# Optimization experiments

Measured on AMD Instinct MI355X. Metric: run time of the kernel, lower is better.

## Reference

```python
import jax, jax.numpy as jnp
import numpy as np

B, H, S, D = 2, 16, 2048, 64

def setup_inputs() -> dict:
    key = jax.random.key(0)
    kq, kk, kv = jax.random.split(key, 3)
    q = jax.random.normal(kq, (B, H, S, D), dtype=jnp.float32)
    k = jax.random.normal(kk, (B, H, S, D), dtype=jnp.float32)
    v = jax.random.normal(kv, (B, H, S, D), dtype=jnp.float32)
    # additive causal mask: 0 on/below diagonal, -1e9 above
    causal = jnp.tril(jnp.ones((S, S), dtype=bool))
    mask = jnp.where(causal, 0.0, -1e9).astype(jnp.float32)[None, None]
    return {"q": q, "k": k, "v": v, "mask": mask}

def reference(q, k, v, mask):
    # scores: [B,H,Sq,Sk]
    scale = 1.0 / jnp.sqrt(jnp.asarray(k.shape[-1], dtype=q.dtype))
    scores = jnp.einsum("bhqd,bhkd->bhqk", q, k) * scale
    scores = scores + mask
    attn = jax.nn.softmax(scores, axis=-1)
    return jnp.einsum("bhqk,bhkd->bhqd", attn, v)
```

## Files before the change

### kernel.cpp

```cpp
#include <hip/hip_runtime.h>
#include <hip/hip_bf16.h>


#define S_LEN 2048
#define D_DIM 64
#define BKV 64
#define NBH 32
#define NT128 16

typedef __bf16 bf16x8 __attribute__((ext_vector_type(8)));
typedef __bf16 bf16x4 __attribute__((ext_vector_type(4)));
typedef float f32x4 __attribute__((ext_vector_type(4)));

#define QSCALE 0.1803368801111243f
#define NEG_MASK (-1e30f)
#define M_INIT  (-1e29f)
#define THRLOG2 11.5f

__device__ inline void glds16(const void* g, void* l) {
    __builtin_amdgcn_global_load_lds(
        (const __attribute__((address_space(1))) unsigned int*)g,
        (__attribute__((address_space(3))) unsigned int*)l, 16, 0, 0);
}

__device__ inline float m3(float a, float b, float c) {
    return fmaxf(fmaxf(a, b), c);
}

__global__ __launch_bounds__(256)
void conv_fused_kernel(const float* __restrict__ k, const float* __restrict__ v,
                       __bf16* __restrict__ kb, __bf16* __restrict__ vt)
{
    __shared__ __bf16 T[64][72];
    const int bh = blockIdx.y, st = blockIdx.x;
    const int tid = threadIdx.x;
    const size_t base = (size_t)bh * S_LEN * D_DIM + (size_t)st * 64 * D_DIM;
    const float* kh = k + base;
    const float* vh = v + base;
    __bf16* kbh = kb + base;

#pragma unroll
    for (int it = 0; it < 2; ++it) {
        size_t i = ((size_t)tid + it * 256) * 8;
        float4 a = *(const float4*)(kh + i);
        float4 b = *(const float4*)(kh + i + 4);
        bf16x8 o;
        o[0] = (__bf16)a.x; o[1] = (__bf16)a.y; o[2] = (__bf16)a.z; o[3] = (__bf16)a.w;
        o[4] = (__bf16)b.x; o[5] = (__bf16)b.y; o[6] = (__bf16)b.z; o[7] = (__bf16)b.w;
        *(bf16x8*)(kbh + i) = o;
    }

#pragma unroll
    for (int it = 0; it < 4; ++it) {
        int idx = tid + it * 256;
        int s = idx >> 4, c4 = idx & 15;
        float4 f = *(const float4*)(vh + s * D_DIM + c4 * 4);
        T[c4 * 4 + 0][s] = (__bf16)f.x;
        T[c4 * 4 + 1][s] = (__bf16)f.y;
        T[c4 * 4 + 2][s] = (__bf16)f.z;
        T[c4 * 4 + 3][s] = (__bf16)f.w;
    }
    __syncthreads();
    __bf16* vth = vt + (size_t)bh * D_DIM * S_LEN + st * 64;
#pragma unroll
    for (int it = 0; it < 2; ++it) {
        int idx = tid + it * 256;
        int d = idx >> 3, c8 = idx & 7;
        int kk = c8 >> 2, g = c8 & 3;
        bf16x4 v0 = *(const bf16x4*)&T[d][kk * 32 + 4 * g];
        bf16x4 v1 = *(const bf16x4*)&T[d][kk * 32 + 16 + 4 * g];
        bf16x8 o;
        o[0] = v0[0]; o[1] = v0[1]; o[2] = v0[2]; o[3] = v0[3];
        o[4] = v1[0]; o[5] = v1[1]; o[6] = v1[2]; o[7] = v1[3];
        *(bf16x8*)(vth + (size_t)d * S_LEN + c8 * 8) = o;
    }
}


#define STAGE(kt, buf)                                                          \
    {                                                                           \
        _Pragma("unroll")                                                       \
        for (int u = 0; u < 2; ++u) {                                           \
            glds16(kh + (size_t)((kt) * BKV + row_u[u]) * D_DIM + scol_u[u],    \
                   (__bf16*)&KL[buf][0][0] + (u * 4 + w) * 512);                \
            glds16(vh + (size_t)row_u[u] * S_LEN + (kt) * BKV + scol_u[u],      \
                   (__bf16*)&VL[buf][0][0] + (u * 4 + w) * 512);                \
        }                                                                       \
    }


__global__ __launch_bounds__(256, 4)
void attn_fwd_split(const float* __restrict__ q, const __bf16* __restrict__ kb,
                    const __bf16* __restrict__ vt, __bf16* __restrict__ opart,
                    float* __restrict__ ml)
{
    __shared__ __bf16 KL[2][64][64];
    __shared__ __bf16 VL[2][64][64];

    const int tid  = threadIdx.x;
    const int w    = tid >> 6;
    const int lane = tid & 63;
    const int l15  = lane & 15;
    const int lg   = lane >> 4;

    const int u0 = blockIdx.x;
    const int T  = NT128 - 1 - (u0 >> 1);
    const int h  = u0 & 1;
    const int bh = blockIdx.y;
    const int qbase = T * 128;
    const int cnt   = T + 1;

    const float*  qh = q  + (size_t)bh * S_LEN * D_DIM;
    const __bf16* kh = kb + (size_t)bh * S_LEN * D_DIM;
    const __bf16* vh = vt + (size_t)bh * D_DIM * S_LEN;

    int row_u[2], scol_u[2];
#pragma unroll
    for (int u = 0; u < 2; ++u) {
        int e = (u * 4 + w) * 512 + lane * 8;
        int r = e >> 6, c0 = e & 63;
        row_u[u]  = r;
        scol_u[u] = c0 ^ ((r & 7) << 3);
    }

    bf16x8 qf[2][2];
#pragma unroll
    for (int qc = 0; qc < 2; ++qc) {
        const int qrow = qbase + w * 32 + qc * 16 + l15;
        const float* qp = qh + (size_t)qrow * D_DIM + 8 * lg;
#pragma unroll
        for (int kk = 0; kk < 2; ++kk) {
            float4 a = *(const float4*)(qp + kk * 32);
            float4 b = *(const float4*)(qp + kk * 32 + 4);
            bf16x8 f;
            f[0] = (__bf16)(a.x * QSCALE); f[1] = (__bf16)(a.y * QSCALE);
            f[2] = (__bf16)(a.z * QSCALE); f[3] = (__bf16)(a.w * QSCALE);
            f[4] = (__bf16)(b.x * QSCALE); f[5] = (__bf16)(b.y * QSCALE);
            f[6] = (__bf16)(b.z * QSCALE); f[7] = (__bf16)(b.w * QSCALE);
            qf[qc][kk] = f;
        }
    }

    f32x4 acc[4][2] = {};
    float m_run[2]  = {M_INIT, M_INIT};
    float l_part[2] = {0.0f, 0.0f};

    STAGE(h, 0);

    for (int i = 0; i < cnt; ++i) {
        const int kt  = h + 2 * i;
        const int cur = i & 1;
        asm volatile("s_waitcnt vmcnt(0)" ::: "memory");
        __builtin_amdgcn_s_barrier();
        if (i + 1 < cnt) STAGE(kt + 2, cur ^ 1);

        bf16x8 kf[4][2];
#pragma unroll
        for (int jt = 0; jt < 4; ++jt) {
            const int j  = jt * 16 + l15;
            const int sw = (j & 7) << 3;
            kf[jt][0] = *(const bf16x8*)&KL[cur][j][(8 * lg) ^ sw];
            kf[jt][1] = *(const bf16x8*)&KL[cur][j][(32 + 8 * lg) ^ sw];
        }

        f32x4 s0[4], s1[4];
        __builtin_amdgcn_s_setprio(1);
#pragma unroll
        for (int jt = 0; jt < 4; ++jt) {
            f32x4 c = {};
            c = __builtin_amdgcn_mfma_f32_16x16x32_bf16(kf[jt][0], qf[0][0], c, 0, 0, 0);
            c = __builtin_amdgcn_mfma_f32_16x16x32_bf16(kf[jt][1], qf[0][1], c, 0, 0, 0);
            s0[jt] = c;
            f32x4 d = {};
            d = __builtin_amdgcn_mfma_f32_16x16x32_bf16(kf[jt][0], qf[1][0], d, 0, 0, 0);
            d = __builtin_amdgcn_mfma_f32_16x16x32_bf16(kf[jt][1], qf[1][1], d, 0, 0, 0);
            s1[jt] = d;
        }
        __builtin_amdgcn_s_setprio(0);

        if (i == cnt - 1) {
            const int q0 = w * 32 + l15;
#pragma unroll
            for (int jt = 0; jt < 4; ++jt)
#pragma unroll
                for (int r = 0; r < 4; ++r) {
                    const int jl = h * 64 + jt * 16 + 4 * lg + r;
                    if (jl > q0)      s0[jt][r] = NEG_MASK;
                    if (jl > q0 + 16) s1[jt][r] = NEG_MASK;
                }
        }

        float mxl0, mxl1;
        {
            float t0 = m3(s0[0][0], s0[0][1], s0[0][2]);
            float t1 = m3(s0[0][3], s0[1][0], s0[1][1]);
            float t2 = m3(s0[1][2], s0[1][3], s0[2][0]);
            float t3 = m3(s0[2][1], s0[2][2], s0[2][3]);
            float t4 = m3(s0[3][0], s0[3][1], s0[3][2]);
            mxl0 = m3(m3(t0, t1, t2), m3(t3, t4, s0[3][3]), NEG_MASK);
            float u1 = m3(s1[0][0], s1[0][1], s1[0][2]);
            float u2 = m3(s1[0][3], s1[1][0], s1[1][1]);
            float u3 = m3(s1[1][2], s1[1][3], s1[2][0]);
            float u4 = m3(s1[2][1], s1[2][2], s1[2][3]);
            float u5 = m3(s1[3][0], s1[3][1], s1[3][2]);
            mxl1 = m3(m3(u1, u2, u3), m3(u4, u5, s1[3][3]), NEG_MASK);
        }

        if (__any((mxl0 > m_run[0] + THRLOG2) || (mxl1 > m_run[1] + THRLOG2))) {
            float mx0 = fmaxf(mxl0, __shfl_xor(mxl0, 16));
            mx0 = fmaxf(mx0, __shfl_xor(mx0, 32));
            float mx1 = fmaxf(mxl1, __shfl_xor(mxl1, 16));
            mx1 = fmaxf(mx1, __shfl_xor(mx1, 32));
            const float mt0 = fmaxf(m_run[0], mx0);
            const float mt1 = fmaxf(m_run[1], mx1);
            const float c0 = __builtin_amdgcn_exp2f(m_run[0] - mt0);
            const float c1 = __builtin_amdgcn_exp2f(m_run[1] - mt1);
            l_part[0] *= c0; m_run[0] = mt0;
            l_part[1] *= c1; m_run[1] = mt1;
            float ca0[4], ca1[4];
#pragma unroll
            for (int r = 0; r < 4; ++r) {
                ca0[r] = __shfl(c0, 4 * lg + r);
                ca1[r] = __shfl(c1, 4 * lg + r);
            }
#pragma unroll
            for (int dt = 0; dt < 4; ++dt)
#pragma unroll
                for (int r = 0; r < 4; ++r) {
                    acc[dt][0][r] *= ca0[r];
                    acc[dt][1][r] *= ca1[r];
                }
        }

        float ps0 = 0.0f, ps1 = 0.0f;
        bf16x8 pa0[2], pa1[2];
#pragma unroll
        for (int kk = 0; kk < 2; ++kk)
#pragma unroll
            for (int i2 = 0; i2 < 4; ++i2) {
                float ea = __builtin_amdgcn_exp2f(s0[2 * kk][i2] - m_run[0]);
                float eb = __builtin_amdgcn_exp2f(s0[2 * kk + 1][i2] - m_run[0]);
                ps0 += ea + eb;
                pa0[kk][i2]     = (__bf16)ea;
                pa0[kk][4 + i2] = (__bf16)eb;
                float fa = __builtin_amdgcn_exp2f(s1[2 * kk][i2] - m_run[1]);
                float fb = __builtin_amdgcn_exp2f(s1[2 * kk + 1][i2] - m_run[1]);
                ps1 += fa + fb;
                pa1[kk][i2]     = (__bf16)fa;
                pa1[kk][4 + i2] = (__bf16)fb;
            }
        l_part[0] += ps0;
        l_part[1] += ps1;

        __builtin_amdgcn_s_setprio(1);
#pragma unroll
        for (int dt = 0; dt < 4; ++dt) {
            const int d  = dt * 16 + l15;
            const int sw = (d & 7) << 3;
#pragma unroll
            for (int kk = 0; kk < 2; ++kk) {
                bf16x8 vb = *(const bf16x8*)&VL[cur][d][(kk * 32 + 8 * lg) ^ sw];
                acc[dt][0] = __builtin_amdgcn_mfma_f32_16x16x32_bf16(pa0[kk], vb, acc[dt][0], 0, 0, 0);
                acc[dt][1] = __builtin_amdgcn_mfma_f32_16x16x32_bf16(pa1[kk], vb, acc[dt][1], 0, 0, 0);
            }
        }
        __builtin_amdgcn_s_setprio(0);
    }

    __bf16* op  = opart + ((((size_t)bh * NT128 + T) * 2 + h) << 13);
    float*  mlp = ml    + ((((size_t)bh * NT128 + T) * 2 + h) << 8);
#pragma unroll
    for (int qc = 0; qc < 2; ++qc) {
        float lt = l_part[qc] + __shfl_xor(l_part[qc], 16);
        lt += __shfl_xor(lt, 32);
#pragma unroll
        for (int dt = 0; dt < 4; ++dt)
#pragma unroll
            for (int r = 0; r < 4; ++r)
                op[(w * 32 + qc * 16 + 4 * lg + r) * 64 + dt * 16 + l15] =
                    (__bf16)acc[dt][qc][r];
        if (lg == 0) {
            mlp[w * 32 + qc * 16 + l15]       = m_run[qc];
            mlp[128 + w * 32 + qc * 16 + l15] = lt;
        }
    }
}


__global__ __launch_bounds__(256)
void combine_kernel(const __bf16* __restrict__ opart, const float* __restrict__ ml,
                    float* __restrict__ out)
{
    const int T   = blockIdx.x;
    const int bh  = blockIdx.y;
    const int tid = threadIdx.x;
    const int row = tid >> 1;
    const int c0  = (tid & 1) * 32;

    const float* mlp = ml + (((size_t)bh * NT128 + T) * 2 << 8);
    const float m0 = mlp[row],       l0 = mlp[128 + row];
    const float m1 = mlp[256 + row], l1 = mlp[384 + row];
    const float M  = fmaxf(m0, m1);
    const float w0 = __builtin_amdgcn_exp2f(m0 - M);
    const float w1 = __builtin_amdgcn_exp2f(m1 - M);
    const float li = __builtin_amdgcn_rcpf(w0 * l0 + w1 * l1);

    const __bf16* o0 = opart + (((size_t)bh * NT128 + T) * 2 << 13) + row * 64 + c0;
    const __bf16* o1 = o0 + 8192;
    float* oh = out + ((size_t)bh * S_LEN + T * 128 + row) * D_DIM + c0;
#pragma unroll
    for (int cc = 0; cc < 4; ++cc) {
        bf16x8 a = *(const bf16x8*)(o0 + cc * 8);
        bf16x8 b = *(const bf16x8*)(o1 + cc * 8);
        float4 r0, r1;
        r0.x = ((float)a[0] * w0 + (float)b[0] * w1) * li;
        r0.y = ((float)a[1] * w0 + (float)b[1] * w1) * li;
        r0.z = ((float)a[2] * w0 + (float)b[2] * w1) * li;
        r0.w = ((float)a[3] * w0 + (float)b[3] * w1) * li;
        r1.x = ((float)a[4] * w0 + (float)b[4] * w1) * li;
        r1.y = ((float)a[5] * w0 + (float)b[5] * w1) * li;
        r1.z = ((float)a[6] * w0 + (float)b[6] * w1) * li;
        r1.w = ((float)a[7] * w0 + (float)b[7] * w1) * li;
        ((float4*)(oh + cc * 8))[0] = r0;
        ((float4*)(oh + cc * 8))[1] = r1;
    }
}


__global__ __launch_bounds__(256)
void attn_fwd_glds(const float* __restrict__ q, const __bf16* __restrict__ kb,
                   const __bf16* __restrict__ vt, float* __restrict__ out)
{
    __shared__ __bf16 KL[3][64][64];
    __shared__ __bf16 VL[3][64][64];

    const int tid  = threadIdx.x;
    const int w    = tid >> 6;
    const int lane = tid & 63;
    const int l15  = lane & 15;
    const int lg   = lane >> 4;

    const int p  = blockIdx.x;
    const int bh = blockIdx.y;

    const float*  qh = q  + (size_t)bh * S_LEN * D_DIM;
    const __bf16* kh = kb + (size_t)bh * S_LEN * D_DIM;
    const __bf16* vh = vt + (size_t)bh * D_DIM * S_LEN;
    float*        oh = out + (size_t)bh * S_LEN * D_DIM;

    int row_u[2], scol_u[2];
#pragma unroll
    for (int u = 0; u < 2; ++u) {
        int e = (u * 4 + w) * 512 + lane * 8;
        int r = e >> 6, c0 = e & 63;
        row_u[u]  = r;
        scol_u[u] = c0 ^ ((r & 7) << 3);
    }

    for (int half = 0; half < 2; ++half) {
        const int qtile = (half == 0) ? (31 - p) : p;
        const int qbase = qtile * 64;
        const int nt    = qtile + 1;

        bf16x8 qf[2];
        {
            const int qrow = qbase + w * 16 + l15;
            const float* qp = qh + (size_t)qrow * D_DIM + 8 * lg;
#pragma unroll
            for (int kk = 0; kk < 2; ++kk) {
                float4 a = *(const float4*)(qp + kk * 32);
                float4 b = *(const float4*)(qp + kk * 32 + 4);
                bf16x8 f;
                f[0] = (__bf16)(a.x * QSCALE); f[1] = (__bf16)(a.y * QSCALE);
                f[2] = (__bf16)(a.z * QSCALE); f[3] = (__bf16)(a.w * QSCALE);
                f[4] = (__bf16)(b.x * QSCALE); f[5] = (__bf16)(b.y * QSCALE);
                f[6] = (__bf16)(b.z * QSCALE); f[7] = (__bf16)(b.w * QSCALE);
                qf[kk] = f;
            }
        }

        f32x4 acc[4] = {};
        float m_run = M_INIT;
        float l_part = 0.0f;

        if (half == 1) __syncthreads();
        STAGE(0, 0);
        if (nt > 1) STAGE(1, 1);

        for (int kt = 0; kt < nt; ++kt) {
            const int cur = kt % 3;
            if (kt + 1 < nt) { asm volatile("s_waitcnt vmcnt(4)" ::: "memory"); }
            else             { asm volatile("s_waitcnt vmcnt(0)" ::: "memory"); }
            __builtin_amdgcn_s_barrier();
            if (kt + 2 < nt) STAGE(kt + 2, (kt + 2) % 3);

            f32x4 s[4];
            __builtin_amdgcn_s_setprio(1);
#pragma unroll
            for (int jt = 0; jt < 4; ++jt) {
                const int j  = jt * 16 + l15;
                const int sw = (j & 7) << 3;
                f32x4 c = {};
#pragma unroll
                for (int kk = 0; kk < 2; ++kk) {
                    bf16x8 kf = *(const bf16x8*)&KL[cur][j][(kk * 32 + 8 * lg) ^ sw];
                    c = __builtin_amdgcn_mfma_f32_16x16x32_bf16(kf, qf[kk], c, 0, 0, 0);
                }
                s[jt] = c;
// ... 163 lines not shown
            sfrag[kc] = c;
        }

        if (kt == qtile) {
#pragma unroll
            for (int kc = 0; kc < 4; ++kc) {
                const int j = kv0 + kc * 16 + l15;
#pragma unroll
                for (int r = 0; r < 4; ++r) {
                    const int qrow = qbase + w * 16 + lg * 4 + r;
                    if (j > qrow) sfrag[kc][r] = -1e30f;
                }
            }
        }

        float mt[4], corr[4], ps[4];
#pragma unroll
        for (int r = 0; r < 4; ++r) {
            float mx = fmaxf(fmaxf(sfrag[0][r], sfrag[1][r]),
                             fmaxf(sfrag[2][r], sfrag[3][r]));
            mx = fmaxf(mx, __shfl_xor(mx, 1));
            mx = fmaxf(mx, __shfl_xor(mx, 2));
            mx = fmaxf(mx, __shfl_xor(mx, 4));
            mx = fmaxf(mx, __shfl_xor(mx, 8));
            mt[r]   = fmaxf(m_run[r], mx);
            corr[r] = __expf(m_run[r] - mt[r]);
            ps[r]   = 0.0f;
        }
#pragma unroll
        for (int kc = 0; kc < 4; ++kc) {
#pragma unroll
            for (int r = 0; r < 4; ++r) {
                float pp = __expf(sfrag[kc][r] - mt[r]);
                ps[r] += pp;
                Plds[w][lg * 4 + r][kc * 16 + l15] = (__bf16)pp;
            }
        }
#pragma unroll
        for (int r = 0; r < 4; ++r) {
            ps[r] += __shfl_xor(ps[r], 1);
            ps[r] += __shfl_xor(ps[r], 2);
            ps[r] += __shfl_xor(ps[r], 4);
            ps[r] += __shfl_xor(ps[r], 8);
            l_run[r] = l_run[r] * corr[r] + ps[r];
            m_run[r] = mt[r];
        }
#pragma unroll
        for (int dt = 0; dt < 4; ++dt)
#pragma unroll
            for (int r = 0; r < 4; ++r)
                acc[dt][r] *= corr[r];

#pragma unroll
        for (int kk = 0; kk < 2; ++kk) {
            bf16x8 pf = *(const bf16x8*)&Plds[w][l15][kk * 32 + 8 * lg];
#pragma unroll
            for (int dt = 0; dt < 4; ++dt) {
                bf16x8 vf = *(const bf16x8*)&Vt[dt * 16 + l15][kk * 32 + 8 * lg];
                acc[dt] = __builtin_amdgcn_mfma_f32_16x16x32_bf16(pf, vf, acc[dt], 0, 0, 0);
            }
        }
    }

#pragma unroll
    for (int dt = 0; dt < 4; ++dt) {
#pragma unroll
        for (int r = 0; r < 4; ++r) {
            const int qrow = qbase + w * 16 + lg * 4 + r;
            oh[(size_t)qrow * D_DIM + dt * 16 + l15] = acc[dt][r] / l_run[r];
        }
    }
}

extern "C" void kernel_launch(void* const* d_in, const int* in_sizes, int n_in,
                              void* d_out, int out_size, void* d_ws, size_t ws_size,
                              hipStream_t stream) {
    const float* q = (const float*)d_in[0];
    const float* k = (const float*)d_in[1];
    const float* v = (const float*)d_in[2];
    float* out = (float*)d_out;

    const size_t kv_elems   = (size_t)NBH * S_LEN * D_DIM;
    const size_t conv_bytes = kv_elems * 2 * sizeof(__bf16);
    const size_t op_bytes   = (size_t)NBH * NT128 * 2 * 8192 * 2;
    const size_t ml_bytes   = (size_t)NBH * NT128 * 2 * 256 * 4;

    if (ws_size >= conv_bytes + op_bytes + ml_bytes) {
        __bf16* kb = (__bf16*)d_ws;
        __bf16* vt = kb + kv_elems;
        __bf16* opart = (__bf16*)((char*)d_ws + conv_bytes);
        float*  ml    = (float*)((char*)d_ws + conv_bytes + op_bytes);
        conv_fused_kernel<<<dim3(S_LEN / 64, NBH), dim3(256), 0, stream>>>(k, v, kb, vt);
        attn_fwd_split<<<dim3(32, NBH), dim3(256), 0, stream>>>(q, kb, vt, opart, ml);
        combine_kernel<<<dim3(NT128, NBH), dim3(256), 0, stream>>>(opart, ml, out);
    } else if (ws_size >= conv_bytes) {
        __bf16* kb = (__bf16*)d_ws;
        __bf16* vt = kb + kv_elems;
        conv_fused_kernel<<<dim3(S_LEN / 64, NBH), dim3(256), 0, stream>>>(k, v, kb, vt);
        attn_fwd_glds<<<dim3(16, NBH), dim3(256), 0, stream>>>(q, kb, vt, out);
    } else {
        attn_fwd_fallback<<<dim3(S_LEN / 64, NBH), dim3(256), 0, stream>>>(q, k, v, out);
    }
}
```

Measured before the change: 65.00 us.

## Split KV four ways and pair mirrored query tiles per block for balance

The split-KV attention kernel now divides each query tile's causal key range into four interleaved chunks instead of two. Each block walks two query tiles in turn, a long one (15-p) and a short one (p), so causal work is spread evenly across blocks and the longest block finishes sooner. The causal mask now applies to any diagonal key tile rather than only the last iteration, and the combine kernel merges four partial results per row. In exchange, the bf16 partial-output and max/sum workspace doubles, which adds global memory traffic and needs a larger workspace. If the workspace is too small, the code drops to the slower fallback path.

After: 88.69 us. +36.5%, slower.

```diff
diff --git a/kernel.cpp b/kernel.cpp
--- a/kernel.cpp
+++ b/kernel.cpp
@@ -104,11 +104,9 @@
     const int lg   = lane >> 4;
 
     const int u0 = blockIdx.x;
-    const int T  = NT128 - 1 - (u0 >> 1);
-    const int h  = u0 & 1;
+    const int p  = u0 >> 2;
+    const int h  = u0 & 3;
     const int bh = blockIdx.y;
-    const int qbase = T * 128;
-    const int cnt   = T + 1;
 
     const float*  qh = q  + (size_t)bh * S_LEN * D_DIM;
     const __bf16* kh = kb + (size_t)bh * S_LEN * D_DIM;
@@ -123,165 +121,173 @@
         scol_u[u] = c0 ^ ((r & 7) << 3);
     }
 
-    bf16x8 qf[2][2];
-#pragma unroll
-    for (int qc = 0; qc < 2; ++qc) {
-        const int qrow = qbase + w * 32 + qc * 16 + l15;
-        const float* qp = qh + (size_t)qrow * D_DIM + 8 * lg;
-#pragma unroll
-        for (int kk = 0; kk < 2; ++kk) {
-            float4 a = *(const float4*)(qp + kk * 32);
-            float4 b = *(const float4*)(qp + kk * 32 + 4);
-            bf16x8 f;
-            f[0] = (__bf16)(a.x * QSCALE); f[1] = (__bf16)(a.y * QSCALE);
-            f[2] = (__bf16)(a.z * QSCALE); f[3] = (__bf16)(a.w * QSCALE);
-            f[4] = (__bf16)(b.x * QSCALE); f[5] = (__bf16)(b.y * QSCALE);
-            f[6] = (__bf16)(b.z * QSCALE); f[7] = (__bf16)(b.w * QSCALE);
-            qf[qc][kk] = f;
-        }
-    }
-
-    f32x4 acc[4][2] = {};
-    float m_run[2]  = {M_INIT, M_INIT};
-    float l_part[2] = {0.0f, 0.0f};
-
-    STAGE(h, 0);
-
-    for (int i = 0; i < cnt; ++i) {
-        const int kt  = h + 2 * i;
-        const int cur = i & 1;
-        asm volatile("s_waitcnt vmcnt(0)" ::: "memory");
-        __builtin_amdgcn_s_barrier();
-        if (i + 1 < cnt) STAGE(kt + 2, cur ^ 1);
-
-        bf16x8 kf[4][2];
-#pragma unroll
-        for (int jt = 0; jt < 4; ++jt) {
-            const int j  = jt * 16 + l15;
-            const int sw = (j & 7) << 3;
-            kf[jt][0] = *(const bf16x8*)&KL[cur][j][(8 * lg) ^ sw];
-            kf[jt][1] = *(const bf16x8*)&KL[cur][j][(32 + 8 * lg) ^ sw];
-        }
-
-        f32x4 s0[4], s1[4];
-        __builtin_amdgcn_s_setprio(1);
-#pragma unroll
-        for (int jt = 0; jt < 4; ++jt) {
-            f32x4 c = {};
-            c = __builtin_amdgcn_mfma_f32_16x16x32_bf16(kf[jt][0], qf[0][0], c, 0, 0, 0);
-            c = __builtin_amdgcn_mfma_f32_16x16x32_bf16(kf[jt][1], qf[0][1], c, 0, 0, 0);
-            s0[jt] = c;
-            f32x4 d = {};
-            d = __builtin_amdgcn_mfma_f32_16x16x32_bf16(kf[jt][0], qf[1][0], d, 0, 0, 0);
-            d = __builtin_amdgcn_mfma_f32_16x16x32_bf16(kf[jt][1], qf[1][1], d, 0, 0, 0);
-            s1[jt] = d;
-        }
-        __builtin_amdgcn_s_setprio(0);
-
-        if (i == cnt - 1) {
-            const int q0 = w * 32 + l15;
-#pragma unroll
-            for (int jt = 0; jt < 4; ++jt)
+    for (int chain = 0; chain < 2; ++chain) {
+        const int T     = (chain == 0) ? (NT128 - 1 - p) : p;
+        const int qbase = T * 128;
+        const int cnt   = (2 * T + 1 >= h) ? ((2 * T + 1 - h) >> 2) + 1 : 0;
+
+        bf16x8 qf[2][2];
+#pragma unroll
+        for (int qc = 0; qc < 2; ++qc) {
+            const int qrow = qbase + w * 32 + qc * 16 + l15;
+            const float* qp = qh + (size_t)qrow * D_DIM + 8 * lg;
+#pragma unroll
+            for (int kk = 0; kk < 2; ++kk) {
+                float4 a = *(const float4*)(qp + kk * 32);
+                float4 b = *(const float4*)(qp + kk * 32 + 4);
+                bf16x8 f;
+                f[0] = (__bf16)(a.x * QSCALE); f[1] = (__bf16)(a.y * QSCALE);
+                f[2] = (__bf16)(a.z * QSCALE); f[3] = (__bf16)(a.w * QSCALE);
+                f[4] = (__bf16)(b.x * QSCALE); f[5] = (__bf16)(b.y * QSCALE);
+                f[6] = (__bf16)(b.z * QSCALE); f[7] = (__bf16)(b.w * QSCALE);
+                qf[qc][kk] = f;
+            }
+        }
+
+        f32x4 acc[4][2] = {};
+        float m_run[2]  = {M_INIT, M_INIT};
+        float l_part[2] = {0.0f, 0.0f};
+
+        if (chain == 1) __syncthreads();
+        if (cnt > 0) STAGE(h, 0);
+
+        for (int i = 0; i < cnt; ++i) {
+            const int kt  = h + 4 * i;
+            const int cur = i & 1;
+            asm volatile("s_waitcnt vmcnt(0)" ::: "memory");
+            __builtin_amdgcn_s_barrier();
+            if (i + 1 < cnt) STAGE(kt + 4, cur ^ 1);
+
+            bf16x8 kf[4][2];
+#pragma unroll
+            for (int jt = 0; jt < 4; ++jt) {
+                const int j  = jt * 16 + l15;
+                const int sw = (j & 7) << 3;
+                kf[jt][0] = *(const bf16x8*)&KL[cur][j][(8 * lg) ^ sw];
+                kf[jt][1] = *(const bf16x8*)&KL[cur][j][(32 + 8 * lg) ^ sw];
+            }
+
+            f32x4 s0[4], s1[4];
+            __builtin_amdgcn_s_setprio(1);
+#pragma unroll
+            for (int jt = 0; jt < 4; ++jt) {
+                f32x4 c = {};
+                c = __builtin_amdgcn_mfma_f32_16x16x32_bf16(kf[jt][0], qf[0][0], c, 0, 0, 0);
+                c = __builtin_amdgcn_mfma_f32_16x16x32_bf16(kf[jt][1], qf[0][1], c, 0, 0, 0);
+                s0[jt] = c;
+                f32x4 d = {};
+                d = __builtin_amdgcn_mfma_f32_16x16x32_bf16(kf[jt][0], qf[1][0], d, 0, 0, 0);
+                d = __builtin_amdgcn_mfma_f32_16x16x32_bf16(kf[jt][1], qf[1][1], d, 0, 0, 0);
+                s1[jt] = d;
+            }
+            __builtin_amdgcn_s_setprio(0);
+
+            if (kt >= 2 * T) {
+                const int dj = (kt - 2 * T) * 64;
+                const int q0 = w * 32 + l15;
+#pragma unroll
+                for (int jt = 0; jt < 4; ++jt)
+#pragma unroll
+                    for (int r = 0; r < 4; ++r) {
+                        const int jl = dj + jt * 16 + 4 * lg + r;
+                        if (jl > q0)      s0[jt][r] = NEG_MASK;
+                        if (jl > q0 + 16) s1[jt][r] = NEG_MASK;
+                    }
+            }
+
+            float mxl0, mxl1;
+            {
+                float t0 = m3(s0[0][0], s0[0][1], s0[0][2]);
+                float t1 = m3(s0[0][3], s0[1][0], s0[1][1]);
+                float t2 = m3(s0[1][2], s0[1][3], s0[2][0]);
+                float t3 = m3(s0[2][1], s0[2][2], s0[2][3]);
+                float t4 = m3(s0[3][0], s0[3][1], s0[3][2]);
+                mxl0 = m3(m3(t0, t1, t2), m3(t3, t4, s0[3][3]), NEG_MASK);
+                float u1 = m3(s1[0][0], s1[0][1], s1[0][2]);
+                float u2 = m3(s1[0][3], s1[1][0], s1[1][1]);
+                float u3 = m3(s1[1][2], s1[1][3], s1[2][0]);
+                float u4 = m3(s1[2][1], s1[2][2], s1[2][3]);
+                float u5 = m3(s1[3][0], s1[3][1], s1[3][2]);
+                mxl1 = m3(m3(u1, u2, u3), m3(u4, u5, s1[3][3]), NEG_MASK);
+            }
+
+            if (__any((mxl0 > m_run[0] + THRLOG2) || (mxl1 > m_run[1] + THRLOG2))) {
+                float mx0 = fmaxf(mxl0, __shfl_xor(mxl0, 16));
+                mx0 = fmaxf(mx0, __shfl_xor(mx0, 32));
+                float mx1 = fmaxf(mxl1, __shfl_xor(mxl1, 16));
+                mx1 = fmaxf(mx1, __shfl_xor(mx1, 32));
+                const float mt0 = fmaxf(m_run[0], mx0);
+                const float mt1 = fmaxf(m_run[1], mx1);
+                const float c0 = __builtin_amdgcn_exp2f(m_run[0] - mt0);
+                const float c1 = __builtin_amdgcn_exp2f(m_run[1] - mt1);
+                l_part[0] *= c0; m_run[0] = mt0;
+                l_part[1] *= c1; m_run[1] = mt1;
+                float ca0[4], ca1[4];
 #pragma unroll
                 for (int r = 0; r < 4; ++r) {
-                    const int jl = h * 64 + jt * 16 + 4 * lg + r;
-                    if (jl > q0)      s0[jt][r] = NEG_MASK;
-                    if (jl > q0 + 16) s1[jt][r] = NEG_MASK;
-                }
-        }
-
-        float mxl0, mxl1;
-        {
-            float t0 = m3(s0[0][0], s0[0][1], s0[0][2]);
-            float t1 = m3(s0[0][3], s0[1][0], s0[1][1]);
-            float t2 = m3(s0[1][2], s0[1][3], s0[2][0]);
-            float t3 = m3(s0[2][1], s0[2][2], s0[2][3]);
-            float t4 = m3(s0[3][0], s0[3][1], s0[3][2]);
-            mxl0 = m3(m3(t0, t1, t2), m3(t3, t4, s0[3][3]), NEG_MASK);
-            float u1 = m3(s1[0][0], s1[0][1], s1[0][2]);
-            float u2 = m3(s1[0][3], s1[1][0], s1[1][1]);
-            float u3 = m3(s1[1][2], s1[1][3], s1[2][0]);
-            float u4 = m3(s1[2][1], s1[2][2], s1[2][3]);
-            float u5 = m3(s1[3][0], s1[3][1], s1[3][2]);
-            mxl1 = m3(m3(u1, u2, u3), m3(u4, u5, s1[3][3]), NEG_MASK);
-        }
-
-        if (__any((mxl0 > m_run[0] + THRLOG2) || (mxl1 > m_run[1] + THRLOG2))) {
-            float mx0 = fmaxf(mxl0, __shfl_xor(mxl0, 16));
-            mx0 = fmaxf(mx0, __shfl_xor(mx0, 32));
-            float mx1 = fmaxf(mxl1, __shfl_xor(mxl1, 16));
-            mx1 = fmaxf(mx1, __shfl_xor(mx1, 32));
-            const float mt0 = fmaxf(m_run[0], mx0);
-            const float mt1 = fmaxf(m_run[1], mx1);
-            const float c0 = __builtin_amdgcn_exp2f(m_run[0] - mt0);
-            const float c1 = __builtin_amdgcn_exp2f(m_run[1] - mt1);
-            l_part[0] *= c0; m_run[0] = mt0;
-            l_part[1] *= c1; m_run[1] = mt1;
-            float ca0[4], ca1[4];
-#pragma unroll
-            for (int r = 0; r < 4; ++r) {
-                ca0[r] = __shfl(c0, 4 * lg + r);
-                ca1[r] = __shfl(c1, 4 * lg + r);
-            }
+                    ca0[r] = __shfl(c0, 4 * lg + r);
+                    ca1[r] = __shfl(c1, 4 * lg + r);
+                }
+#pragma unroll
+                for (int dt = 0; dt < 4; ++dt)
+#pragma unroll
+                    for (int r = 0; r < 4; ++r) {
+                        acc[dt][0][r] *= ca0[r];
+                        acc[dt][1][r] *= ca1[r];
+                    }
+            }
+
+            float ps0 = 0.0f, ps1 = 0.0f;
+            bf16x8 pa0[2], pa1[2];
+#pragma unroll
+            for (int kk = 0; kk < 2; ++kk)
+#pragma unroll
+                for (int i2 = 0; i2 < 4; ++i2) {
+                    float ea = __builtin_amdgcn_exp2f(s0[2 * kk][i2] - m_run[0]);
+                    float eb = __builtin_amdgcn_exp2f(s0[2 * kk + 1][i2] - m_run[0]);
+                    ps0 += ea + eb;
+                    pa0[kk][i2]     = (__bf16)ea;
+                    pa0[kk][4 + i2] = (__bf16)eb;
+                    float fa = __builtin_amdgcn_exp2f(s1[2 * kk][i2] - m_run[1]);
+                    float fb = __builtin_amdgcn_exp2f(s1[2 * kk + 1][i2] - m_run[1]);
+                    ps1 += fa + fb;
+                    pa1[kk][i2]     = (__bf16)fa;
+                    pa1[kk][4 + i2] = (__bf16)fb;
+                }
+            l_part[0] += ps0;
+            l_part[1] += ps1;
+
+            __builtin_amdgcn_s_setprio(1);
+#pragma unroll
+            for (int dt = 0; dt < 4; ++dt) {
+                const int d  = dt * 16 + l15;
+                const int sw = (d & 7) << 3;
+#pragma unroll
+                for (int kk = 0; kk < 2; ++kk) {
+                    bf16x8 vb = *(const bf16x8*)&VL[cur][d][(kk * 32 + 8 * lg) ^ sw];
+                    acc[dt][0] = __builtin_amdgcn_mfma_f32_16x16x32_bf16(pa0[kk], vb, acc[dt][0], 0, 0, 0);
+                    acc[dt][1] = __builtin_amdgcn_mfma_f32_16x16x32_bf16(pa1[kk], vb, acc[dt][1], 0, 0, 0);
+                }
+            }
+            __builtin_amdgcn_s_setprio(0);
+        }
+
+        __bf16* op  = opart + ((((size_t)bh * NT128 + T) * 4 + h) << 13);
+        float*  mlp = ml    + ((((size_t)bh * NT128 + T) * 4 + h) << 8);
+#pragma unroll
+        for (int qc = 0; qc < 2; ++qc) {
+            float lt = l_part[qc] + __shfl_xor(l_part[qc], 16);
+            lt += __shfl_xor(lt, 32);
 #pragma unroll
             for (int dt = 0; dt < 4; ++dt)
 #pragma unroll
-                for (int r = 0; r < 4; ++r) {
-                    acc[dt][0][r] *= ca0[r];
-                    acc[dt][1][r] *= ca1[r];
-                }
-        }
-
-        float ps0 = 0.0f, ps1 = 0.0f;
-        bf16x8 pa0[2], pa1[2];
-#pragma unroll
-        for (int kk = 0; kk < 2; ++kk)
-#pragma unroll
-            for (int i2 = 0; i2 < 4; ++i2) {
-                float ea = __builtin_amdgcn_exp2f(s0[2 * kk][i2] - m_run[0]);
-                float eb = __builtin_amdgcn_exp2f(s0[2 * kk + 1][i2] - m_run[0]);
-                ps0 += ea + eb;
-                pa0[kk][i2]     = (__bf16)ea;
-                pa0[kk][4 + i2] = (__bf16)eb;
-                float fa = __builtin_amdgcn_exp2f(s1[2 * kk][i2] - m_run[1]);
-                float fb = __builtin_amdgcn_exp2f(s1[2 * kk + 1][i2] - m_run[1]);
-                ps1 += fa + fb;
-                pa1[kk][i2]     = (__bf16)fa;
-                pa1[kk][4 + i2] = (__bf16)fb;
-            }
-        l_part[0] += ps0;
-        l_part[1] += ps1;
-
-        __builtin_amdgcn_s_setprio(1);
-#pragma unroll
-        for (int dt = 0; dt < 4; ++dt) {
-            const int d  = dt * 16 + l15;
-            const int sw = (d & 7) << 3;
-#pragma unroll
-            for (int kk = 0; kk < 2; ++kk) {
-                bf16x8 vb = *(const bf16x8*)&VL[cur][d][(kk * 32 + 8 * lg) ^ sw];
-                acc[dt][0] = __builtin_amdgcn_mfma_f32_16x16x32_bf16(pa0[kk], vb, acc[dt][0], 0, 0, 0);
-                acc[dt][1] = __builtin_amdgcn_mfma_f32_16x16x32_bf16(pa1[kk], vb, acc[dt][1], 0, 0, 0);
-            }
-        }
-        __builtin_amdgcn_s_setprio(0);
-    }
-
-    __bf16* op  = opart + ((((size_t)bh * NT128 + T) * 2 + h) << 13);
-    float*  mlp = ml    + ((((size_t)bh * NT128 + T) * 2 + h) << 8);
-#pragma unroll
-    for (int qc = 0; qc < 2; ++qc) {
-        float lt = l_part[qc] + __shfl_xor(l_part[qc], 16);
-        lt += __shfl_xor(lt, 32);
-#pragma unroll
-        for (int dt = 0; dt < 4; ++dt)
-#pragma unroll
-            for (int r = 0; r < 4; ++r)
-                op[(w * 32 + qc * 16 + 4 * lg + r) * 64 + dt * 16 + l15] =
-                    (__bf16)acc[dt][qc][r];
-        if (lg == 0) {
-            mlp[w * 32 + qc * 16 + l15]       = m_run[qc];
-            mlp[128 + w * 32 + qc * 16 + l15] = lt;
+                for (int r = 0; r < 4; ++r)
+                    op[(w * 32 + qc * 16 + 4 * lg + r) * 64 + dt * 16 + l15] =
+                        (__bf16)acc[dt][qc][r];
+            if (lg == 0) {
+                mlp[w * 32 + qc * 16 + l15]       = m_run[qc];
+                mlp[128 + w * 32 + qc * 16 + l15] = lt;
+            }
         }
     }
 }
@@ -297,33 +303,43 @@
     const int row = tid >> 1;
     const int c0  = (tid & 1) * 32;
 
-    const float* mlp = ml + (((size_t)bh * NT128 + T) * 2 << 8);
-    const float m0 = mlp[row],       l0 = mlp[128 + row];
-    const float m1 = mlp[256 + row], l1 = mlp[384 + row];
-    const float M  = fmaxf(m0, m1);
-    const float w0 = __builtin_amdgcn_exp2f(m0 - M);
-    const float w1 = __builtin_amdgcn_exp2f(m1 - M);
-    const float li = __builtin_amdgcn_rcpf(w0 * l0 + w1 * l1);
-
-    const __bf16* o0 = opart + (((size_t)bh * NT128 + T) * 2 << 13) + row * 64 + c0;
-    const __bf16* o1 = o0 + 8192;
+    const float* mlp = ml + ((((size_t)bh * NT128 + T) * 4) << 8);
+    float m[4], l[4];
+#pragma unroll
+    for (int hh = 0; hh < 4; ++hh) {
+        m[hh] = mlp[hh * 256 + row];
+        l[hh] = mlp[hh * 256 + 128 + row];
+    }
+    const float M = fmaxf(fmaxf(m[0], m[1]), fmaxf(m[2], m[3]));
+    float wgt[4], L = 0.0f;
+#pragma unroll
+    for (int hh = 0; hh < 4; ++hh) {
+        wgt[hh] = __builtin_amdgcn_exp2f(m[hh] - M);
+        L += wgt[hh] * l[hh];
+    }
+    const float li = __builtin_amdgcn_rcpf(L);
+
+    const __bf16* ob = opart + ((((size_t)bh * NT128 + T) * 4) << 13) + row * 64 + c0;
     float* oh = out + ((size_t)bh * S_LEN + T * 128 + row) * D_DIM + c0;
-#pragma unroll
-    for (int cc = 0; cc < 4; ++cc) {
-        bf16x8 a = *(const bf16x8*)(o0 + cc * 8);
-        bf16x8 b = *(const bf16x8*)(o1 + cc * 8);
-        float4 r0, r1;
-        r0.x = ((float)a[0] * w0 + (float)b[0] * w1) * li;
-        r0.y = ((float)a[1] * w0 + (float)b[1] * w1) * li;
-        r0.z = ((float)a[2] * w0 + (float)b[2] * w1) * li;
-        r0.w = ((float)a[3] * w0 + (float)b[3] * w1) * li;
-        r1.x = ((float)a[4] * w0 + (float)b[4] * w1) * li;
-        r1.y = ((float)a[5] * w0 + (float)b[5] * w1) * li;
-        r1.z = ((float)a[6] * w0 + (float)b[6] * w1) * li;
-        r1.w = ((float)a[7] * w0 + (float)b[7] * w1) * li;
-        ((float4*)(oh + cc * 8))[0] = r0;
-        ((float4*)(oh + cc * 8))[1] = r1;
-    }
+
+    float res[32];
+#pragma unroll
+    for (int j = 0; j < 32; ++j) res[j] = 0.0f;
+#pragma unroll
+    for (int hh = 0; hh < 4; ++hh) {
+        const __bf16* o = ob + hh * 8192;
+#pragma unroll
+        for (int cc = 0; cc < 4; ++cc) {
+            bf16x8 a = *(const bf16x8*)(o + cc * 8);
+#pragma unroll
+            for (int j = 0; j < 8; ++j)
+                res[cc * 8 + j] += (float)a[j] * wgt[hh];
+        }
+    }
+#pragma unroll
+    for (int cc = 0; cc < 8; ++cc)
+        ((float4*)oh)[cc] = make_float4(res[cc*4] * li, res[cc*4+1] * li,
+                                        res[cc*4+2] * li, res[cc*4+3] * li);
 }
 
 
@@ -653,8 +669,8 @@
 
     const size_t kv_elems   = (size_t)NBH * S_LEN * D_DIM;
     const size_t conv_bytes = kv_elems * 2 * sizeof(__bf16);
-    const size_t op_bytes   = (size_t)NBH * NT128 * 2 * 8192 * 2;
-    const size_t ml_bytes   = (size_t)NBH * NT128 * 2 * 256 * 4;
+    const size_t op_bytes   = (size_t)NBH * NT128 * 4 * 8192 * 2;
+    const size_t ml_bytes   = (size_t)NBH * NT128 * 4 * 256 * 4;
 
     if (ws_size >= conv_bytes + op_bytes + ml_bytes) {
         __bf16* kb = (__bf16*)d_ws;
```

## Pair causal query tiles per block and triple-buffer KV in split attention

Applied to the files above, without the earlier changes.

Each split-attention block now handles two query tiles in sequence, a long one (T=15-p) and a short one (T=p), so every block does the same amount of causal work. The grid shrinks from 32 to 16 blocks along x. K/V staging moves from double to triple buffering with partial vmcnt waits, and the occupancy hint in launch bounds is dropped. The partial output is written in an MFMA-native fragment layout with vectorized stores, and the combine kernel is rewritten to read that layout. The risks are half as many blocks to fill the CUs and more LDS per block, which can lower occupancy.

Measured after the change: 59.95 us. -7.8%, faster.

```diff
diff --git a/kernel.cpp b/kernel.cpp
--- a/kernel.cpp
+++ b/kernel.cpp
@@ -89,13 +89,13 @@
     }
 
 
-__global__ __launch_bounds__(256, 4)
+__global__ __launch_bounds__(256)
 void attn_fwd_split(const float* __restrict__ q, const __bf16* __restrict__ kb,
                     const __bf16* __restrict__ vt, __bf16* __restrict__ opart,
                     float* __restrict__ ml)
 {
-    __shared__ __bf16 KL[2][64][64];
-    __shared__ __bf16 VL[2][64][64];
+    __shared__ __bf16 KL[3][64][64];
+    __shared__ __bf16 VL[3][64][64];
 
     const int tid  = threadIdx.x;
     const int w    = tid >> 6;
@@ -104,11 +104,9 @@
     const int lg   = lane >> 4;
 
     const int u0 = blockIdx.x;
-    const int T  = NT128 - 1 - (u0 >> 1);
+    const int p  = u0 >> 1;
     const int h  = u0 & 1;
     const int bh = blockIdx.y;
-    const int qbase = T * 128;
-    const int cnt   = T + 1;
 
     const float*  qh = q  + (size_t)bh * S_LEN * D_DIM;
     const __bf16* kh = kb + (size_t)bh * S_LEN * D_DIM;
@@ -123,165 +121,181 @@
         scol_u[u] = c0 ^ ((r & 7) << 3);
     }
 
-    bf16x8 qf[2][2];
-#pragma unroll
-    for (int qc = 0; qc < 2; ++qc) {
-        const int qrow = qbase + w * 32 + qc * 16 + l15;
-        const float* qp = qh + (size_t)qrow * D_DIM + 8 * lg;
-#pragma unroll
-        for (int kk = 0; kk < 2; ++kk) {
-            float4 a = *(const float4*)(qp + kk * 32);
-            float4 b = *(const float4*)(qp + kk * 32 + 4);
-            bf16x8 f;
-            f[0] = (__bf16)(a.x * QSCALE); f[1] = (__bf16)(a.y * QSCALE);
-            f[2] = (__bf16)(a.z * QSCALE); f[3] = (__bf16)(a.w * QSCALE);
-            f[4] = (__bf16)(b.x * QSCALE); f[5] = (__bf16)(b.y * QSCALE);
-            f[6] = (__bf16)(b.z * QSCALE); f[7] = (__bf16)(b.w * QSCALE);
-            qf[qc][kk] = f;
-        }
-    }
-
-    f32x4 acc[4][2] = {};
-    float m_run[2]  = {M_INIT, M_INIT};
-    float l_part[2] = {0.0f, 0.0f};
-
-    STAGE(h, 0);
-
-    for (int i = 0; i < cnt; ++i) {
-        const int kt  = h + 2 * i;
-        const int cur = i & 1;
-        asm volatile("s_waitcnt vmcnt(0)" ::: "memory");
-        __builtin_amdgcn_s_barrier();
-        if (i + 1 < cnt) STAGE(kt + 2, cur ^ 1);
-
-        bf16x8 kf[4][2];
-#pragma unroll
-        for (int jt = 0; jt < 4; ++jt) {
-            const int j  = jt * 16 + l15;
-            const int sw = (j & 7) << 3;
-            kf[jt][0] = *(const bf16x8*)&KL[cur][j][(8 * lg) ^ sw];
-            kf[jt][1] = *(const bf16x8*)&KL[cur][j][(32 + 8 * lg) ^ sw];
-        }
-
-        f32x4 s0[4], s1[4];
-        __builtin_amdgcn_s_setprio(1);
-#pragma unroll
-        for (int jt = 0; jt < 4; ++jt) {
-            f32x4 c = {};
-            c = __builtin_amdgcn_mfma_f32_16x16x32_bf16(kf[jt][0], qf[0][0], c, 0, 0, 0);
-            c = __builtin_amdgcn_mfma_f32_16x16x32_bf16(kf[jt][1], qf[0][1], c, 0, 0, 0);
-            s0[jt] = c;
-            f32x4 d = {};
-            d = __builtin_amdgcn_mfma_f32_16x16x32_bf16(kf[jt][0], qf[1][0], d, 0, 0, 0);
-            d = __builtin_amdgcn_mfma_f32_16x16x32_bf16(kf[jt][1], qf[1][1], d, 0, 0, 0);
-            s1[jt] = d;
-        }
-        __builtin_amdgcn_s_setprio(0);
-
-        if (i == cnt - 1) {
-            const int q0 = w * 32 + l15;
-#pragma unroll
-            for (int jt = 0; jt < 4; ++jt)
+    for (int chain = 0; chain < 2; ++chain) {
+        const int T     = (chain == 0) ? (NT128 - 1 - p) : p;
+        const int qbase = T * 128;
+        const int cnt   = T + 1;
+
+        bf16x8 qf[2][2];
+#pragma unroll
+        for (int qc = 0; qc < 2; ++qc) {
+            const int qrow = qbase + w * 32 + qc * 16 + l15;
+            const float* qp = qh + (size_t)qrow * D_DIM + 8 * lg;
+#pragma unroll
+            for (int kk = 0; kk < 2; ++kk) {
+                float4 a = *(const float4*)(qp + kk * 32);
+                float4 b = *(const float4*)(qp + kk * 32 + 4);
+                bf16x8 f;
+                f[0] = (__bf16)(a.x * QSCALE); f[1] = (__bf16)(a.y * QSCALE);
+                f[2] = (__bf16)(a.z * QSCALE); f[3] = (__bf16)(a.w * QSCALE);
+                f[4] = (__bf16)(b.x * QSCALE); f[5] = (__bf16)(b.y * QSCALE);
+                f[6] = (__bf16)(b.z * QSCALE); f[7] = (__bf16)(b.w * QSCALE);
+                qf[qc][kk] = f;
+            }
+        }
+
+        f32x4 acc[4][2] = {};
+        float m_run[2]  = {M_INIT, M_INIT};
+        float l_part[2] = {0.0f, 0.0f};
+
+        if (chain == 1) __syncthreads();
+        STAGE(h, 0);
+        if (cnt > 1) STAGE(h + 2, 1);
+
+        for (int i = 0; i < cnt; ++i) {
+            const int cur = i % 3;
+            if (i + 1 < cnt) { asm volatile("s_waitcnt vmcnt(4)" ::: "memory"); }
+            else             { asm volatile("s_waitcnt vmcnt(0)" ::: "memory"); }
+            __builtin_amdgcn_s_barrier();
+            if (i + 2 < cnt) STAGE(h + 2 * (i + 2), (i + 2) % 3);
+
+            bf16x8 kf[4][2];
+#pragma unroll
+            for (int jt = 0; jt < 4; ++jt) {
+                const int j  = jt * 16 + l15;
+                const int sw = (j & 7) << 3;
+                kf[jt][0] = *(const bf16x8*)&KL[cur][j][(8 * lg) ^ sw];
+                kf[jt][1] = *(const bf16x8*)&KL[cur][j][(32 + 8 * lg) ^ sw];
+            }
+
+            f32x4 s0[4], s1[4];
+            __builtin_amdgcn_s_setprio(1);
+#pragma unroll
+            for (int jt = 0; jt < 4; ++jt) {
+                f32x4 c = {};
+                c = __builtin_amdgcn_mfma_f32_16x16x32_bf16(kf[jt][0], qf[0][0], c, 0, 0, 0);
+                c = __builtin_amdgcn_mfma_f32_16x16x32_bf16(kf[jt][1], qf[0][1], c, 0, 0, 0);
+                s0[jt] = c;
+                f32x4 d = {};
+                d = __builtin_amdgcn_mfma_f32_16x16x32_bf16(kf[jt][0], qf[1][0], d, 0, 0, 0);
+                d = __builtin_amdgcn_mfma_f32_16x16x32_bf16(kf[jt][1], qf[1][1], d, 0, 0, 0);
+                s1[jt] = d;
+            }
+            __builtin_amdgcn_s_setprio(0);
+
+            if (i == cnt - 1) {
+                const int q0 = w * 32 + l15;
+#pragma unroll
+                for (int jt = 0; jt < 4; ++jt)
+#pragma unroll
+                    for (int r = 0; r < 4; ++r) {
+                        const int jl = h * 64 + jt * 16 + 4 * lg + r;
+                        if (jl > q0)      s0[jt][r] = NEG_MASK;
+                        if (jl > q0 + 16) s1[jt][r] = NEG_MASK;
+                    }
+            }
+
+            float mxl0, mxl1;
+            {
+                float t0 = m3(s0[0][0], s0[0][1], s0[0][2]);
+                float t1 = m3(s0[0][3], s0[1][0], s0[1][1]);
+                float t2 = m3(s0[1][2], s0[1][3], s0[2][0]);
+                float t3 = m3(s0[2][1], s0[2][2], s0[2][3]);
+                float t4 = m3(s0[3][0], s0[3][1], s0[3][2]);
+                mxl0 = m3(m3(t0, t1, t2), m3(t3, t4, s0[3][3]), NEG_MASK);
+                float u1 = m3(s1[0][0], s1[0][1], s1[0][2]);
+                float u2 = m3(s1[0][3], s1[1][0], s1[1][1]);
+                float u3 = m3(s1[1][2], s1[1][3], s1[2][0]);
+                float u4 = m3(s1[2][1], s1[2][2], s1[2][3]);
+                float u5 = m3(s1[3][0], s1[3][1], s1[3][2]);
+                mxl1 = m3(m3(u1, u2, u3), m3(u4, u5, s1[3][3]), NEG_MASK);
+            }
+
+            if (__any((mxl0 > m_run[0] + THRLOG2) || (mxl1 > m_run[1] + THRLOG2))) {
+                float mx0 = fmaxf(mxl0, __shfl_xor(mxl0, 16));
+                mx0 = fmaxf(mx0, __shfl_xor(mx0, 32));
+                float mx1 = fmaxf(mxl1, __shfl_xor(mxl1, 16));
+                mx1 = fmaxf(mx1, __shfl_xor(mx1, 32));
+                const float mt0 = fmaxf(m_run[0], mx0);
+                const float mt1 = fmaxf(m_run[1], mx1);
+                const float c0 = __builtin_amdgcn_exp2f(m_run[0] - mt0);
+                const float c1 = __builtin_amdgcn_exp2f(m_run[1] - mt1);
+                l_part[0] *= c0; m_run[0] = mt0;
+                l_part[1] *= c1; m_run[1] = mt1;
+                float ca0[4], ca1[4];
 #pragma unroll
                 for (int r = 0; r < 4; ++r) {
-                    const int jl = h * 64 + jt * 16 + 4 * lg + r;
-                    if (jl > q0)      s0[jt][r] = NEG_MASK;
-                    if (jl > q0 + 16) s1[jt][r] = NEG_MASK;
+                    ca0[r] = __shfl(c0, 4 * lg + r);
+                    ca1[r] = __shfl(c1, 4 * lg + r);
                 }
-        }
-
-        float mxl0, mxl1;
-        {
-            float t0 = m3(s0[0][0], s0[0][1], s0[0][2]);
-            float t1 = m3(s0[0][3], s0[1][0], s0[1][1]);
-            float t2 = m3(s0[1][2], s0[1][3], s0[2][0]);
-            float t3 = m3(s0[2][1], s0[2][2], s0[2][3]);
-            float t4 = m3(s0[3][0], s0[3][1], s0[3][2]);
-            mxl0 = m3(m3(t0, t1, t2), m3(t3, t4, s0[3][3]), NEG_MASK);
-            float u1 = m3(s1[0][0], s1[0][1], s1[0][2]);
-            float u2 = m3(s1[0][3], s1[1][0], s1[1][1]);
-            float u3 = m3(s1[1][2], s1[1][3], s1[2][0]);
-            float u4 = m3(s1[2][1], s1[2][2], s1[2][3]);
-            float u5 = m3(s1[3][0], s1[3][1], s1[3][2]);
-            mxl1 = m3(m3(u1, u2, u3), m3(u4, u5, s1[3][3]), NEG_MASK);
-        }
-
-        if (__any((mxl0 > m_run[0] + THRLOG2) || (mxl1 > m_run[1] + THRLOG2))) {
-            float mx0 = fmaxf(mxl0, __shfl_xor(mxl0, 16));
-            mx0 = fmaxf(mx0, __shfl_xor(mx0, 32));
-            float mx1 = fmaxf(mxl1, __shfl_xor(mxl1, 16));
-            mx1 = fmaxf(mx1, __shfl_xor(mx1, 32));
-            const float mt0 = fmaxf(m_run[0], mx0);
-            const float mt1 = fmaxf(m_run[1], mx1);
-            const float c0 = __builtin_amdgcn_exp2f(m_run[0] - mt0);
-            const float c1 = __builtin_amdgcn_exp2f(m_run[1] - mt1);
-            l_part[0] *= c0; m_run[0] = mt0;
-            l_part[1] *= c1; m_run[1] = mt1;
-            float ca0[4], ca1[4];
+#pragma unroll
+                for (int dt = 0; dt < 4; ++dt)
+#pragma unroll
+                    for (int r = 0; r < 4; ++r) {
+                        acc[dt][0][r] *= ca0[r];
+                        acc[dt][1][r] *= ca1[r];
+                    }
+            }
+
+            float ps0 = 0.0f, ps1 = 0.0f;
+            bf16x8 pa0[2], pa1[2];
+#pragma unroll
+            for (int kk = 0; kk < 2; ++kk)
+#pragma unroll
+                for (int i2 = 0; i2 < 4; ++i2) {
+                    float ea = __builtin_amdgcn_exp2f(s0[2 * kk][i2] - m_run[0]);
+                    float eb = __builtin_amdgcn_exp2f(s0[2 * kk + 1][i2] - m_run[0]);
+                    ps0 += ea + eb;
+                    pa0[kk][i2]     = (__bf16)ea;
+                    pa0[kk][4 + i2] = (__bf16)eb;
+                    float fa = __builtin_amdgcn_exp2f(s1[2 * kk][i2] - m_run[1]);
+                    float fb = __builtin_amdgcn_exp2f(s1[2 * kk + 1][i2] - m_run[1]);
+                    ps1 += fa + fb;
+                    pa1[kk][i2]     = (__bf16)fa;
+                    pa1[kk][4 + i2] = (__bf16)fb;
+                }
+            l_part[0] += ps0;
+            l_part[1] += ps1;
+
+            __builtin_amdgcn_s_setprio(1);
+#pragma unroll
+            for (int dt = 0; dt < 4; ++dt) {
+                const int d  = dt * 16 + l15;
+                const int sw = (d & 7) << 3;
+#pragma unroll
+                for (int kk = 0; kk < 2; ++kk) {
+                    bf16x8 vb = *(const bf16x8*)&VL[cur][d][(kk * 32 + 8 * lg) ^ sw];
+                    acc[dt][0] = __builtin_amdgcn_mfma_f32_16x16x32_bf16(pa0[kk], vb, acc[dt][0], 0, 0, 0);
+                    acc[dt][1] = __builtin_amdgcn_mfma_f32_16x16x32_bf16(pa1[kk], vb, acc[dt][1], 0, 0, 0);
+                }
+            }
+            __builtin_amdgcn_s_setprio(0);
+        }
+
+        float lt[2];
+#pragma unroll
+        for (int qc = 0; qc < 2; ++qc) {
+            lt[qc] = l_part[qc] + __shfl_xor(l_part[qc], 16);
+            lt[qc] += __shfl_xor(lt[qc], 32);
+        }
+        __bf16* op = opart + ((((size_t)bh * NT128 + T) * 2 + h) << 13) + (size_t)tid * 32;
+#pragma unroll
+        for (int dt = 0; dt < 4; ++dt) {
+            bf16x8 wv;
 #pragma unroll
             for (int r = 0; r < 4; ++r) {
-                ca0[r] = __shfl(c0, 4 * lg + r);
-                ca1[r] = __shfl(c1, 4 * lg + r);
-            }
-#pragma unroll
-            for (int dt = 0; dt < 4; ++dt)
-#pragma unroll
-                for (int r = 0; r < 4; ++r) {
-                    acc[dt][0][r] *= ca0[r];
-                    acc[dt][1][r] *= ca1[r];
-                }
-        }
-
-        float ps0 = 0.0f, ps1 = 0.0f;
-        bf16x8 pa0[2], pa1[2];
-#pragma unroll
-        for (int kk = 0; kk < 2; ++kk)
-#pragma unroll
-            for (int i2 = 0; i2 < 4; ++i2) {
-                float ea = __builtin_amdgcn_exp2f(s0[2 * kk][i2] - m_run[0]);
-                float eb = __builtin_amdgcn_exp2f(s0[2 * kk + 1][i2] - m_run[0]);
-                ps0 += ea + eb;
-                pa0[kk][i2]     = (__bf16)ea;
-                pa0[kk][4 + i2] = (__bf16)eb;
-                float fa = __builtin_amdgcn_exp2f(s1[2 * kk][i2] - m_run[1]);
-                float fb = __builtin_amdgcn_exp2f(s1[2 * kk + 1][i2] - m_run[1]);
-                ps1 += fa + fb;
-                pa1[kk][i2]     = (__bf16)fa;
-                pa1[kk][4 + i2] = (__bf16)fb;
-            }
-        l_part[0] += ps0;
-        l_part[1] += ps1;
-
-        __builtin_amdgcn_s_setprio(1);
-#pragma unroll
-        for (int dt = 0; dt < 4; ++dt) {
-            const int d  = dt * 16 + l15;
-            const int sw = (d & 7) << 3;
-#pragma unroll
-            for (int kk = 0; kk < 2; ++kk) {
-                bf16x8 vb = *(const bf16x8*)&VL[cur][d][(kk * 32 + 8 * lg) ^ sw];
-                acc[dt][0] = __builtin_amdgcn_mfma_f32_16x16x32_bf16(pa0[kk], vb, acc[dt][0], 0, 0, 0);
-                acc[dt][1] = __builtin_amdgcn_mfma_f32_16x16x32_bf16(pa1[kk], vb, acc[dt][1], 0, 0, 0);
-            }
-        }
-        __builtin_amdgcn_s_setprio(0);
-    }
-
-    __bf16* op  = opart + ((((size_t)bh * NT128 + T) * 2 + h) << 13);
-    float*  mlp = ml    + ((((size_t)bh * NT128 + T) * 2 + h) << 8);
-#pragma unroll
-    for (int qc = 0; qc < 2; ++qc) {
-        float lt = l_part[qc] + __shfl_xor(l_part[qc], 16);
-        lt += __shfl_xor(lt, 32);
-#pragma unroll
-        for (int dt = 0; dt < 4; ++dt)
-#pragma unroll
-            for (int r = 0; r < 4; ++r)
-                op[(w * 32 + qc * 16 + 4 * lg + r) * 64 + dt * 16 + l15] =
-                    (__bf16)acc[dt][qc][r];
+                wv[r]     = (__bf16)acc[dt][0][r];
+                wv[4 + r] = (__bf16)acc[dt][1][r];
+            }
+            *(bf16x8*)(op + dt * 8) = wv;
+        }
+        float* mlp = ml + ((((size_t)bh * NT128 + T) * 2 + h) << 8);
         if (lg == 0) {
-            mlp[w * 32 + qc * 16 + l15]       = m_run[qc];
-            mlp[128 + w * 32 + qc * 16 + l15] = lt;
+#pragma unroll
+            for (int qc = 0; qc < 2; ++qc) {
+                mlp[w * 32 + qc * 16 + l15]       = m_run[qc];
+                mlp[128 + w * 32 + qc * 16 + l15] = lt[qc];
+            }
         }
     }
 }
@@ -294,35 +308,47 @@
     const int T   = blockIdx.x;
     const int bh  = blockIdx.y;
     const int tid = threadIdx.x;
-    const int row = tid >> 1;
-    const int c0  = (tid & 1) * 32;
-
-    const float* mlp = ml + (((size_t)bh * NT128 + T) * 2 << 8);
-    const float m0 = mlp[row],       l0 = mlp[128 + row];
-    const float m1 = mlp[256 + row], l1 = mlp[384 + row];
-    const float M  = fmaxf(m0, m1);
-    const float w0 = __builtin_amdgcn_exp2f(m0 - M);
-    const float w1 = __builtin_amdgcn_exp2f(m1 - M);
-    const float li = __builtin_amdgcn_rcpf(w0 * l0 + w1 * l1);
-
-    const __bf16* o0 = opart + (((size_t)bh * NT128 + T) * 2 << 13) + row * 64 + c0;
+    const int w    = tid >> 6;
+    const int lane = tid & 63;
+    const int l15  = lane & 15;
+    const int lg   = lane >> 4;
+
+    const size_t b0 = ((size_t)bh * NT128 + T) * 2;
+    const __bf16* o0 = opart + (b0 << 13) + (size_t)tid * 32;
     const __bf16* o1 = o0 + 8192;
-    float* oh = out + ((size_t)bh * S_LEN + T * 128 + row) * D_DIM + c0;
-#pragma unroll
-    for (int cc = 0; cc < 4; ++cc) {
-        bf16x8 a = *(const bf16x8*)(o0 + cc * 8);
-        bf16x8 b = *(const bf16x8*)(o1 + cc * 8);
-        float4 r0, r1;
-        r0.x = ((float)a[0] * w0 + (float)b[0] * w1) * li;
-        r0.y = ((float)a[1] * w0 + (float)b[1] * w1) * li;
-        r0.z = ((float)a[2] * w0 + (float)b[2] * w1) * li;
-        r0.w = ((float)a[3] * w0 + (float)b[3] * w1) * li;
-        r1.x = ((float)a[4] * w0 + (float)b[4] * w1) * li;
-        r1.y = ((float)a[5] * w0 + (float)b[5] * w1) * li;
-        r1.z = ((float)a[6] * w0 + (float)b[6] * w1) * li;
-        r1.w = ((float)a[7] * w0 + (float)b[7] * w1) * li;
-        ((float4*)(oh + cc * 8))[0] = r0;
-        ((float4*)(oh + cc * 8))[1] = r1;
+    const float* ml0 = ml + (b0 << 8);
+    const float* ml1 = ml0 + 256;
+
+    float w0a[2][4], w1a[2][4];
+#pragma unroll
+    for (int qc = 0; qc < 2; ++qc)
+#pragma unroll
+        for (int r = 0; r < 4; ++r) {
+            const int row = w * 32 + qc * 16 + 4 * lg + r;
+            const float m0 = ml0[row], l0 = ml0[128 + row];
+            const float m1 = ml1[row], l1 = ml1[128 + row];
+            const float M  = fmaxf(m0, m1);
+            const float e0 = __builtin_amdgcn_exp2f(m0 - M);
+            const float e1 = __builtin_amdgcn_exp2f(m1 - M);
+            const float li = __builtin_amdgcn_rcpf(e0 * l0 + e1 * l1);
+            w0a[qc][r] = e0 * li;
+            w1a[qc][r] = e1 * li;
+        }
+
+    float* oh = out + ((size_t)bh * S_LEN + T * 128) * D_DIM;
+#pragma unroll
+    for (int dt = 0; dt < 4; ++dt) {
+        bf16x8 a = *(const bf16x8*)(o0 + dt * 8);
+        bf16x8 b = *(const bf16x8*)(o1 + dt * 8);
+#pragma unroll
+        for (int qc = 0; qc < 2; ++qc)
+#pragma unroll
+            for (int r = 0; r < 4; ++r) {
+                const int row = w * 32 + qc * 16 + 4 * lg + r;
+                const int j   = qc * 4 + r;
+                oh[(size_t)row * D_DIM + dt * 16 + l15] =
+                    (float)a[j] * w0a[qc][r] + (float)b[j] * w1a[qc][r];
+            }
     }
 }
 
@@ -662,7 +688,7 @@
         __bf16* opart = (__bf16*)((char*)d_ws + conv_bytes);
         float*  ml    = (float*)((char*)d_ws + conv_bytes + op_bytes);
         conv_fused_kernel<<<dim3(S_LEN / 64, NBH), dim3(256), 0, stream>>>(k, v, kb, vt);
-        attn_fwd_split<<<dim3(32, NBH), dim3(256), 0, stream>>>(q, kb, vt, opart, ml);
+        attn_fwd_split<<<dim3(16, NBH), dim3(256), 0, stream>>>(q, kb, vt, opart, ml);
         combine_kernel<<<dim3(NT128, NBH), dim3(256), 0, stream>>>(opart, ml, out);
     } else if (ws_size >= conv_bytes) {
         __bf16* kb = (__bf16*)d_ws;
```
